# Performance work log

Measured on AMD Instinct MI355X. Metric: run time of the kernel, lower is better.

## Reference

```python
import jax, jax.numpy as jnp
import numpy as np
from jax import lax

BLOCK_LEN = 128  # ctx_len 8192 / blocks 64
NEG_INF = -1e9


def setup_inputs() -> dict:
    key = jax.random.key(0)
    ks = jax.random.split(key, 8)
    N, L, Dm = 2, 8192, 4096
    W, H, dh = 1024, 16, 64  # width = d_model*0.25
    s = lambda fan: 1.0 / np.sqrt(fan)
    return {
        "inputs": jax.random.normal(ks[0], (N, L, Dm), jnp.float32),
        "conv_w": jax.random.normal(ks[1], (3, Dm, 3 * W), jnp.float32) * s(3 * Dm),
        "conv_b": jnp.zeros((3 * W,), jnp.float32),
        "wq": jax.random.normal(ks[2], (W, H, dh), jnp.float32) * s(W),
        "bq": jnp.zeros((H, dh), jnp.float32),
        "wk": jax.random.normal(ks[3], (W, H, dh), jnp.float32) * s(W),
        "bk": jnp.zeros((H, dh), jnp.float32),
        "wv": jax.random.normal(ks[4], (W, H, dh), jnp.float32) * s(W),
        "bv": jnp.zeros((H, dh), jnp.float32),
        "wo": jax.random.normal(ks[5], (H, dh, W), jnp.float32) * s(H * dh),
        "bo": jnp.zeros((W,), jnp.float32),
        "proj_w": jax.random.normal(ks[6], (W, Dm), jnp.float32) * s(W),
        "proj_b": jnp.zeros((Dm,), jnp.float32),
    }


def reference(inputs, conv_w, conv_b, wq, bq, wk, bk, wv, bv, wo, bo, proj_w, proj_b):
    N, L, Dm = inputs.shape
    # Conv1D(kernel=3, same padding) producing q,k,v concatenated
    x = lax.conv_general_dilated(
        inputs, conv_w, window_strides=(1,), padding="SAME",
        dimension_numbers=("NWC", "WIO", "NWC")) + conv_b
    q, k, v = jnp.split(x, 3, axis=-1)  # each [N, L, W]
    W_ = q.shape[-1]
    nb = L // BLOCK_LEN
    # row attention: independent causal attention within each block
    q = q.reshape(N * nb, BLOCK_LEN, W_)
    k = k.reshape(N * nb, BLOCK_LEN, W_)
    v = v.reshape(N * nb, BLOCK_LEN, W_)
    dh = wq.shape[-1]
    qh = jnp.einsum("btd,dhe->bthe", q, wq) + bq  # [B, T, H, dh]
    kh = jnp.einsum("btd,dhe->bthe", k, wk) + bk
    vh = jnp.einsum("btd,dhe->bthe", v, wv) + bv
    scale = 1.0 / jnp.sqrt(jnp.asarray(dh, qh.dtype))
    scores = jnp.einsum("bqhe,bkhe->bhqk", qh * scale, kh)
    causal = jnp.tril(jnp.ones((BLOCK_LEN, BLOCK_LEN), bool))
    scores = jnp.where(causal, scores, NEG_INF)
    p = jax.nn.softmax(scores, axis=-1)
    o = jnp.einsum("bhqk,bkhe->bqhe", p, vh)
    o = jnp.einsum("bqhe,hed->bqd", o, wo) + bo  # MHA output projection -> width
    o = o.reshape(N, L, W_)
    return o @ proj_w + proj_b  # final Dense(d_model)
```

## Files before the change

### kernel.cpp

```cpp
#include <hip/hip_runtime.h>
#include <hip/hip_bf16.h>
#include <stdint.h>

typedef __attribute__((ext_vector_type(8))) short short8;
typedef __attribute__((ext_vector_type(4))) float f32x4;

#define AS1 __attribute__((address_space(1)))
#define AS3 __attribute__((address_space(3)))

__device__ __forceinline__ short f2bf(float x) {
    __hip_bfloat16 h = __float2bfloat16(x);
    union { __hip_bfloat16 h; short s; } u; u.h = h; return u.s;
}

__device__ __forceinline__ void gload_lds16(const short* g, short* l) {
    __builtin_amdgcn_global_load_lds((const AS1 void*)g, (AS3 void*)l, 16, 0, 0);
}

#define SBAR()   __builtin_amdgcn_s_barrier()
#define WAITV(N) asm volatile("s_waitcnt vmcnt(" #N ")")
#define SCHED0() __builtin_amdgcn_sched_barrier(0)

__global__ __launch_bounds__(256, 3) void conv3_gemm(
    const short* __restrict__ A,
    const short* __restrict__ BT,
    short* __restrict__ Cout,
    const float* __restrict__ bias)
{
    __shared__ __align__(16) short As[258 * 32];
    __shared__ __align__(16) short Bs[3 * 128 * 32];
    const int tid = threadIdx.x, lane = tid & 63, wid = tid >> 6;
    const int wm = wid >> 1, wn = wid & 1;
    const int m0 = blockIdx.y * 256, n0 = blockIdx.x * 128;
    const size_t arow0 = (size_t)(m0 >> 13) * 8194 + (size_t)(m0 & 8191);
    const short* Abase = A + arow0 * 4096;
    const short* Bbase = BT + (size_t)n0 * 4096;
    const int c15 = lane & 15, g = lane >> 4, g4 = g * 4;
    const int xr0 = (c15 >> 1) & 3;
    const int xr1 = ((c15 + 1) >> 1) & 3;
    const int xr2 = ((c15 + 2) >> 1) & 3;
    const int srow = tid >> 2;
    const int schunk = (((tid & 3) ^ ((tid >> 3) & 3)) * 8);
    const int srowB = wid * 32 + (lane >> 2);
    const int schunkB = (((lane & 3) ^ ((lane >> 3) & 3)) * 8);

#define STAGE(s) do { \
    const int kc_ = (s) * 32; \
    const short* ga_ = Abase + (size_t)srow * 4096 + kc_ + schunk; \
    short* la_ = As + wid * 512; \
    gload_lds16(ga_, la_); \
    gload_lds16(ga_ + (size_t)64 * 4096, la_ + 2048); \
    gload_lds16(ga_ + (size_t)128 * 4096, la_ + 4096); \
    gload_lds16(ga_ + (size_t)192 * 4096, la_ + 6144); \
    if (wid == 3 && lane < 8) \
        gload_lds16(Abase + (size_t)(256 + (lane >> 2)) * 4096 + kc_ + (lane & 3) * 8, \
                    As + 8192); \
    _Pragma("unroll") \
    for (int tp_ = 0; tp_ < 3; ++tp_) { \
        const short* gb_ = Bbase + (size_t)tp_ * 3072 * 4096 \
                           + (size_t)srowB * 4096 + kc_ + schunkB; \
        short* lb_ = Bs + tp_ * 4096 + wid * 1024; \
        gload_lds16(gb_, lb_); \
        gload_lds16(gb_ + (size_t)16 * 4096, lb_ + 512); \
    } \
} while (0)

#define LDA_T(mi, T, XR) (*(const short8*)(As \
    + (wm * 128 + (mi) * 16 + c15 + (T)) * 32 + ((g ^ (XR)) * 8)))
#define LDB_T(tp, nj) (*(const short8*)(Bs + (tp) * 4096 \
    + (wn * 64 + (nj) * 16 + c15) * 32 + ((g ^ xr0) * 8)))

    f32x4 acc[8][4];
    #pragma unroll
    for (int i = 0; i < 8; ++i)
        #pragma unroll
        for (int j = 0; j < 4; ++j)
            acc[i][j] = (f32x4){0.f, 0.f, 0.f, 0.f};

    STAGE(0);

    for (int s = 0; s < 128; ++s) {
        WAITV(0); SBAR(); SCHED0();
        #pragma unroll
        for (int tp = 0; tp < 3; ++tp) {
            const int xr = (tp == 0) ? xr0 : (tp == 1) ? xr1 : xr2;
            short8 b0 = LDB_T(tp, 0), b1 = LDB_T(tp, 1);
            short8 b2f = LDB_T(tp, 2), b3 = LDB_T(tp, 3);
            __builtin_amdgcn_s_setprio(1);
            #pragma unroll
            for (int mi = 0; mi < 8; ++mi) {
                short8 a = LDA_T(mi, tp, xr);
                acc[mi][0] = __builtin_amdgcn_mfma_f32_16x16x32_bf16(a, b0, acc[mi][0], 0, 0, 0);
                acc[mi][1] = __builtin_amdgcn_mfma_f32_16x16x32_bf16(a, b1, acc[mi][1], 0, 0, 0);
                acc[mi][2] = __builtin_amdgcn_mfma_f32_16x16x32_bf16(a, b2f, acc[mi][2], 0, 0, 0);
                acc[mi][3] = __builtin_amdgcn_mfma_f32_16x16x32_bf16(a, b3, acc[mi][3], 0, 0, 0);
            }
            __builtin_amdgcn_s_setprio(0);
        }
        SBAR();
        if (s + 1 < 128) STAGE(s + 1);
    }

    float bv[4];
    #pragma unroll
    for (int nj = 0; nj < 4; ++nj)
        bv[nj] = bias[n0 + wn * 64 + nj * 16 + c15];
    #pragma unroll
    for (int mi = 0; mi < 8; ++mi) {
        #pragma unroll
        for (int r = 0; r < 4; ++r) {
            const size_t row = (size_t)m0 + wm * 128 + mi * 16 + g4 + r;
            #pragma unroll
            for (int nj = 0; nj < 4; ++nj) {
                const int col = n0 + wn * 64 + nj * 16 + c15;
                Cout[row * 3072 + col] = f2bf(acc[mi][nj][r] + bv[nj]);
            }
        }
    }
#undef STAGE
#undef LDA_T
#undef LDB_T
}

template<int MODE, bool F32OUT>
__global__ __launch_bounds__(512, 2) void gemm256(
    const short* __restrict__ A, int lda,
    const short* __restrict__ BT, int ldb,
    void* __restrict__ Cout, int ldc,
    const float* __restrict__ bias, int Ktiles)
{
    __shared__ __align__(16) short As[2 * 2 * 256 * 32];
    __shared__ __align__(16) short Bs[2 * 2 * 256 * 32];
    const int tid = threadIdx.x, lane = tid & 63, wid = tid >> 6;
    const int wm = wid >> 2, wn = wid & 3;
    const int m0 = blockIdx.y * 256, n0 = blockIdx.x * 256;
    const size_t ldaS = (size_t)lda, ldbS = (size_t)ldb;
    const short* Abase0 = A + (size_t)m0 * ldaS;
    const short* Bbase0 = BT + (size_t)n0 * ldbS + ((MODE == 1) ? (m0 & ~1023) : 0);
    const int c15 = lane & 15, g4 = (lane >> 4) * 4;
    const int swz = ((lane >> 4) ^ ((c15 >> 1) & 3)) * 8;
    const int srow = tid >> 2;
    const int schunk = (((tid & 3) ^ ((tid >> 3) & 3)) * 8);

#define STG_A(u, kh, buf) do { \
    const short* g_ = Abase0 + ((u) << 6) + (kh) * 32 + (size_t)srow * ldaS + schunk; \
    short* l_ = As + (buf) * 16384 + (kh) * 8192 + wid * 512; \
    gload_lds16(g_, l_); \
    gload_lds16(g_ + 128 * ldaS, l_ + 4096); \
} while (0)

#define STG_B(u, kh, buf) do { \
    const short* g_ = Bbase0 + ((u) << 6) + (kh) * 32 + (size_t)srow * ldbS + schunk; \
    short* l_ = Bs + (buf) * 16384 + (kh) * 8192 + wid * 512; \
    gload_lds16(g_, l_); \
    gload_lds16(g_ + 128 * ldbS, l_ + 4096); \
} while (0)

#define LDA_(buf, kk, mi) (*(const short8*)(As + (buf) * 16384 + (kk) * 8192 \
                           + (wm * 128 + (mi) * 16 + c15) * 32 + swz))
#define LDB_(buf, kk, nj) (*(const short8*)(Bs + (buf) * 16384 + (kk) * 8192 \
                           + (wn * 64 + (nj) * 16 + c15) * 32 + swz))

#define MFMA4x4(MB) do { \
    __builtin_amdgcn_s_setprio(1); \
    _Pragma("unroll") \
    for (int mi_ = 0; mi_ < 4; ++mi_) \
        _Pragma("unroll") \
        for (int nj_ = 0; nj_ < 4; ++nj_) \
            acc[(MB) + mi_][nj_] = __builtin_amdgcn_mfma_f32_16x16x32_bf16( \
                af[mi_], bf4[nj_], acc[(MB) + mi_][nj_], 0, 0, 0); \
    __builtin_amdgcn_s_setprio(0); \
} while (0)

    f32x4 acc[8][4];
    #pragma unroll
    for (int i = 0; i < 8; ++i)
        #pragma unroll
        for (int j = 0; j < 4; ++j)
            acc[i][j] = (f32x4){0.f, 0.f, 0.f, 0.f};

    STG_A(0, 0, 0); STG_B(0, 0, 0); STG_A(0, 1, 0); STG_B(0, 1, 0);
    WAITV(4); SBAR(); SCHED0();

    for (int t = 0; t < Ktiles; ++t) {
        const int c = t & 1, nb = c ^ 1;
        const bool st = (t + 1 < Ktiles);
        const int u = t + 1;
        short8 af[4], bf4[4];

        #pragma unroll
        for (int mi = 0; mi < 4; ++mi) af[mi] = LDA_(c, 0, mi);
        #pragma unroll
        for (int nj = 0; nj < 4; ++nj) bf4[nj] = LDB_(c, 0, nj);
        if (st) STG_A(u, 0, nb);
        SBAR();
        MFMA4x4(0);
        SBAR();

        #pragma unroll
        for (int mi = 0; mi < 4; ++mi) af[mi] = LDA_(c, 0, 4 + mi);
        if (st) STG_B(u, 0, nb);
        if (st) { WAITV(4); } else { WAITV(0); }
        SBAR(); SCHED0();
        MFMA4x4(4);
        SBAR();

        #pragma unroll
        for (int mi = 0; mi < 4; ++mi) af[mi] = LDA_(c, 1, mi);
        #pragma unroll
        for (int nj = 0; nj < 4; ++nj) bf4[nj] = LDB_(c, 1, nj);
        if (st) STG_A(u, 1, nb);
        SBAR();
        MFMA4x4(0);
        SBAR();

        #pragma unroll
        for (int mi = 0; mi < 4; ++mi) af[mi] = LDA_(c, 1, 4 + mi);
        if (st) STG_B(u, 1, nb);
        if (st) { WAITV(4); } else { WAITV(0); }
        SBAR(); SCHED0();
        MFMA4x4(4);
        SBAR();
    }

    float bv[4];
    #pragma unroll
    for (int nj = 0; nj < 4; ++nj)
        bv[nj] = bias ? bias[n0 + wn * 64 + nj * 16 + c15] : 0.f;
    #pragma unroll
    for (int mi = 0; mi < 8; ++mi) {
        #pragma unroll
        for (int r = 0; r < 4; ++r) {
            const size_t row = (size_t)m0 + wm * 128 + mi * 16 + g4 + r;
            #pragma unroll
            for (int nj = 0; nj < 4; ++nj) {
                const int col = n0 + wn * 64 + nj * 16 + c15;
                const float v = acc[mi][nj][r] + bv[nj];
                if (F32OUT) ((float*)Cout)[row * (size_t)ldc + col] = v;
                else        ((short*)Cout)[row * (size_t)ldc + col] = f2bf(v);
            }
        }
    }
#undef STG_A
#undef STG_B
#undef LDA_
#undef LDB_
#undef MFMA4x4
}

__global__ __launch_bounds__(256) void attn_kernel(
    const short* __restrict__ qkvh, short* __restrict__ obuf)
{
    __shared__ __align__(16) char smem[54272];
    short* qs = (short*)smem;
    short* ks = (short*)smem + 9216;
    short* vt = (short*)(smem + 36864);
    short* ps = (short*)smem;
    short* os = (short*)smem;

    const int tid = threadIdx.x, lane = tid & 63, wid = tid >> 6;
    const int h = blockIdx.x, b = blockIdx.y;
    const size_t base = (size_t)b * 128 * 3072 + (size_t)h * 64;

    for (int i = tid; i < 1024; i += 256) {
        const int row = i >> 3, c8 = i & 7;
        const size_t g = base + (size_t)row * 3072 + c8 * 8;
        *(short8*)(qs + row * 72 + c8 * 8) = *(const short8*)(qkvh + g);
        *(short8*)(ks + row * 72 + c8 * 8) = *(const short8*)(qkvh + g + 1024);
        short8 vv = *(const short8*)(qkvh + g + 2048);
        #pragma unroll
        for (int j = 0; j < 8; ++j) vt[(c8 * 8 + j) * 136 + row] = vv[j];
    }
    __syncthreads();

    const int c15 = lane & 15, g8 = (lane >> 4) * 8, g4 = (lane >> 4) * 4;
    const int r0 = wid * 32;

    f32x4 sacc[2][8];
    #pragma unroll
    for (int mi = 0; mi < 2; ++mi)
        #pragma unroll
        for (int nj = 0; nj < 8; ++nj)
            sacc[mi][nj] = (f32x4){0.f, 0.f, 0.f, 0.f};
    #pragma unroll
    for (int kk = 0; kk < 2; ++kk) {
        short8 aq[2];
        #pragma unroll
        for (int mi = 0; mi < 2; ++mi)
            aq[mi] = *(const short8*)(qs + (r0 + mi * 16 + c15) * 72 + kk * 32 + g8);
        #pragma unroll
        for (int nj = 0; nj < 8; ++nj) {
            short8 bk8 = *(const short8*)(ks + (nj * 16 + c15) * 72 + kk * 32 + g8);
            #pragma unroll
            for (int mi = 0; mi < 2; ++mi)
                sacc[mi][nj] = __builtin_amdgcn_mfma_f32_16x16x32_bf16(
                    aq[mi], bk8, sacc[mi][nj], 0, 0, 0);
        }
    }
    __syncthreads();

    #pragma unroll
    for (int mi = 0; mi < 2; ++mi) {
        #pragma unroll
        for (int r = 0; r < 4; ++r) {
            const int qrow = r0 + mi * 16 + g4 + r;
            float m = -3.0e38f, pv[8];
            #pragma unroll
            for (int nj = 0; nj < 8; ++nj) {
                float s = sacc[mi][nj][r] * 0.125f;
                if (nj * 16 + c15 > qrow) s = -1.0e9f;
                pv[nj] = s; m = fmaxf(m, s);
            }
            #pragma unroll
            for (int off = 8; off >= 1; off >>= 1) m = fmaxf(m, __shfl_xor(m, off));
            float sum = 0.f;
            #pragma unroll
            for (int nj = 0; nj < 8; ++nj) { float p = __expf(pv[nj] - m); pv[nj] = p; sum += p; }
            #pragma unroll
            for (int off = 8; off >= 1; off >>= 1) sum += __shfl_xor(sum, off);
            const float inv = 1.0f / sum;
            #pragma unroll
            for (int nj = 0; nj < 8; ++nj)
                ps[qrow * 136 + nj * 16 + c15] = f2bf(pv[nj] * inv);
        }
    }
    __syncthreads();

    f32x4 oacc[2][4];
    #pragma unroll
    for (int mi = 0; mi < 2; ++mi)
        #pragma unroll
        for (int nj = 0; nj < 4; ++nj)
            oacc[mi][nj] = (f32x4){0.f, 0.f, 0.f, 0.f};
    #pragma unroll
    for (int kt = 0; kt < 4; ++kt) {
        short8 ap[2];
        #pragma unroll
        for (int mi = 0; mi < 2; ++mi)
            ap[mi] = *(const short8*)(ps + (r0 + mi * 16 + c15) * 136 + kt * 32 + g8);
        #pragma unroll
        for (int nj = 0; nj < 4; ++nj) {
            short8 bv8 = *(const short8*)(vt + (nj * 16 + c15) * 136 + kt * 32 + g8);
            #pragma unroll
            for (int mi = 0; mi < 2; ++mi)
                oacc[mi][nj] = __builtin_amdgcn_mfma_f32_16x16x32_bf16(
                    ap[mi], bv8, oacc[mi][nj], 0, 0, 0);
        }
    }
    __syncthreads();

    #pragma unroll
    for (int mi = 0; mi < 2; ++mi)
        #pragma unroll
        for (int r = 0; r < 4; ++r)
            #pragma unroll
            for (int nj = 0; nj < 4; ++nj)
                os[(r0 + mi * 16 + g4 + r) * 72 + nj * 16 + c15] = f2bf(oacc[mi][nj][r]);
    __syncthreads();

    for (int i = tid; i < 1024; i += 256) {
        const int row = i >> 3, c8 = i & 7;
        *(short8*)(obuf + (size_t)b * 128 * 1024 + (size_t)h * 64
                   + (size_t)row * 1024 + c8 * 8) =
            *(const short8*)(os + row * 72 + c8 * 8);
    }
}

__global__ void pad_convert_inputs(const float* __restrict__ in, short* __restrict__ out)
{
    const int row = blockIdx.x;
    const int n = row / 8194, l = row % 8194;
    short* orow = out + (size_t)row * 4096;
    if (l == 0 || l == 8193) {
        for (int i = threadIdx.x; i < 512; i += 256) {
            uint4 z; z.x = z.y = z.z = z.w = 0u;
            *(uint4*)(orow + i * 8) = z;
        }
    } else {
        const float* irow = in + ((size_t)n * 8192 + (l - 1)) * 4096;
        for (int i = threadIdx.x; i < 512; i += 256) {
            float4 a = *(const float4*)(irow + i * 8);
            float4 b = *(const float4*)(irow + i * 8 + 4);
            short8 v;
            v[0] = f2bf(a.x); v[1] = f2bf(a.y); v[2] = f2bf(a.z); v[3] = f2bf(a.w);
            v[4] = f2bf(b.x); v[5] = f2bf(b.y); v[6] = f2bf(b.z); v[7] = f2bf(b.w);
            *(short8*)(orow + i * 8) = v;
        }
    }
}

__global__ void transpose_convert(const float* __restrict__ in, short* __restrict__ out,
                                  int R, int C)
{
    __shared__ float tile[32][33];
    const int tx = threadIdx.x & 31, ty = threadIdx.x >> 5;
    const int bx = blockIdx.x * 32, by = blockIdx.y * 32;
    #pragma unroll
    for (int i = 0; i < 32; i += 8)
        tile[ty + i][tx] = in[(size_t)(by + ty + i) * C + bx + tx];
    __syncthreads();
    #pragma unroll
    for (int i = 0; i < 32; i += 8)
        out[(size_t)(bx + ty + i) * R + by + tx] = f2bf(tile[tx][ty + i]);
}

__global__ void convert_bf16(const float* __restrict__ in, short* __restrict__ out, int n8)
{
    const int idx = blockIdx.x * 256 + threadIdx.x;
    if (idx < n8) {
        float4 a = *(const float4*)(in + (size_t)idx * 8);
        float4 b = *(const float4*)(in + (size_t)idx * 8 + 4);
        short8 v;
        v[0] = f2bf(a.x); v[1] = f2bf(a.y); v[2] = f2bf(a.z); v[3] = f2bf(a.w);
        v[4] = f2bf(b.x); v[5] = f2bf(b.y); v[6] = f2bf(b.z); v[7] = f2bf(b.w);
        *(short8*)(out + (size_t)idx * 8) = v;
    }
}

__global__ void fuse_bias(const float* __restrict__ bo, const float* __restrict__ projw,
                          const float* __restrict__ projb, float* __restrict__ outb)
{
    const int j = blockIdx.x * 256 + threadIdx.x;
    float s = projb[j];
    for (int w = 0; w < 1024; ++w) s = fmaf(bo[w], projw[(size_t)w * 4096 + j], s);
    outb[j] = s;
}

__global__ void fuse_bias_qkv(const float* __restrict__ conv_b,
                              const float* __restrict__ wq, const float* __restrict__ bq,
                              const float* __restrict__ wk, const float* __restrict__ bk,
                              const float* __restrict__ wv, const float* __restrict__ bv,
                              float* __restrict__ outb)
{
    const int o = blockIdx.x * 256 + threadIdx.x;
    const int p = o >> 10, e = o & 1023;
    const float* w = (p == 0) ? wq : (p == 1) ? wk : wv;
    const float* bb = (p == 0) ? bq : (p == 1) ? bk : bv;
    const float* cb = conv_b + p * 1024;
    float s = bb[e];
    for (int d = 0; d < 1024; ++d) s = fmaf(cb[d], w[(size_t)d * 1024 + e], s);
    outb[o] = s;
}

extern "C" void kernel_launch(void* const* d_in, const int* in_sizes, int n_in,
                              void* d_out, int out_size, void* d_ws, size_t ws_size,
                              hipStream_t stream)
{
    const float* inputs = (const float*)d_in[0];
    const float* conv_w = (const float*)d_in[1];
    const float* conv_b = (const float*)d_in[2];
    const float* wq     = (const float*)d_in[3];
    const float* bq     = (const float*)d_in[4];
    const float* wk     = (const float*)d_in[5];
    const float* bk     = (const float*)d_in[6];
    const float* wv     = (const float*)d_in[7];
    const float* bv     = (const float*)d_in[8];
    const float* wo     = (const float*)d_in[9];
    const float* bo     = (const float*)d_in[10];
    const float* proj_w = (const float*)d_in[11];
    const float* proj_b = (const float*)d_in[12];

    char* ws = (char*)d_ws;
    short* in_pad = (short*)(ws + 0);
    short* cw_bf  = (short*)(ws + 134283264);
    short* qkvh   = (short*)(ws + 134283264);
    short* W2T    = (short*)(ws + 234946560);
    short* wq_t   = (short*)(ws + 310444032);
    short* wo_bf  = (short*)(ws + 316735488);
    short* proj_t = (short*)(ws + 318832640);
    short* WfT    = (short*)(ws + 327221248);
    float* bfused = (float*)(ws + 335609856);
    float* b2     = (float*)(ws + 335626240);
    short* o_buf  = (short*)(ws + 0);

    dim3 blk(256), blk5(512);

    pad_convert_inputs<<<16388, blk, 0, stream>>>(inputs, in_pad);
    convert_bf16<<<18432, blk, 0, stream>>>(conv_w, cw_bf, 4718592);
    transpose_convert<<<dim3(32, 32), blk, 0, stream>>>(wq, wq_t, 1024, 1024);
    transpose_convert<<<dim3(32, 32), blk, 0, stream>>>(wk, wq_t + 1048576, 1024, 1024);
    transpose_convert<<<dim3(32, 32), blk, 0, stream>>>(wv, wq_t + 2097152, 1024, 1024);
    transpose_convert<<<dim3(128, 32), blk, 0, stream>>>(proj_w, proj_t, 1024, 4096);
    convert_bf16<<<512, blk, 0, stream>>>(wo, wo_bf, 131072);
    fuse_bias<<<16, blk, 0, stream>>>(bo, proj_w, proj_b, bfused);
    fuse_bias_qkv<<<12, blk, 0, stream>>>(conv_b, wq, bq, wk, bk, wv, bv, b2);

    gemm256<0, false><<<dim3(4, 16), blk5, 0, stream>>>(
        proj_t, 1024, wo_bf, 1024, WfT, 1024, nullptr, 16);
    for (int t = 0; t < 3; ++t)
        gemm256<1, false><<<dim3(16, 12), blk5, 0, stream>>>(
            wq_t, 1024, cw_bf + (size_t)t * 4096 * 3072, 3072,
            W2T + (size_t)t * 3072 * 4096, 4096, nullptr, 16);
    conv3_gemm<<<dim3(24, 64), blk, 0, stream>>>(in_pad, W2T, qkvh, b2);

    attn_kernel<<<dim3(16, 128), blk, 0, stream>>>(qkvh, o_buf);

    gemm256<0, true><<<dim3(16, 64), blk5, 0, stream>>>(
        o_buf, 1024, WfT, 1024, d_out, 4096, bfused, 16);
}
```

Baseline: 1.494 ms.

## Replace 256x256 double-buffered GEMM with 256x128 single-buffered 4-wave GEMM

The 512-thread, 256x256-tile, double-buffered GEMM is replaced by a 256-thread kernel with 256x128 tiles and a single LDS buffer per 32-wide K step. Each step waits for the load, computes 32 MFMAs per wave, then issues the next load, so load and compute no longer overlap inside a block. The aim is smaller LDS use, more blocks in flight and more tiles for load balance, with latency hidden by other resident blocks rather than the software pipeline. The risks are exposed load latency and more global traffic for B from the narrower N tile.

```diff
diff --git a/kernel.cpp b/kernel.cpp
--- a/kernel.cpp
+++ b/kernel.cpp
@@ -123,54 +123,43 @@
 }
 
 template<int MODE, bool F32OUT>
-__global__ __launch_bounds__(512, 2) void gemm256(
+__global__ __launch_bounds__(256, 3) void gemm128(
     const short* __restrict__ A, int lda,
     const short* __restrict__ BT, int ldb,
     void* __restrict__ Cout, int ldc,
-    const float* __restrict__ bias, int Ktiles)
-{
-    __shared__ __align__(16) short As[2 * 2 * 256 * 32];
-    __shared__ __align__(16) short Bs[2 * 2 * 256 * 32];
+    const float* __restrict__ bias, int Ksteps)
+{
+    __shared__ __align__(16) short As[256 * 32];
+    __shared__ __align__(16) short Bs[128 * 32];
     const int tid = threadIdx.x, lane = tid & 63, wid = tid >> 6;
-    const int wm = wid >> 2, wn = wid & 3;
-    const int m0 = blockIdx.y * 256, n0 = blockIdx.x * 256;
+    const int wm = wid >> 1, wn = wid & 1;
+    const int m0 = blockIdx.y * 256, n0 = blockIdx.x * 128;
     const size_t ldaS = (size_t)lda, ldbS = (size_t)ldb;
-    const short* Abase0 = A + (size_t)m0 * ldaS;
-    const short* Bbase0 = BT + (size_t)n0 * ldbS + ((MODE == 1) ? (m0 & ~1023) : 0);
-    const int c15 = lane & 15, g4 = (lane >> 4) * 4;
-    const int swz = ((lane >> 4) ^ ((c15 >> 1) & 3)) * 8;
+    const short* Abase = A + (size_t)m0 * ldaS;
+    const short* Bbase = BT + (size_t)n0 * ldbS + ((MODE == 1) ? (m0 & ~1023) : 0);
+    const int c15 = lane & 15, g = lane >> 4, g4 = g * 4;
+    const int xr0 = (c15 >> 1) & 3;
     const int srow = tid >> 2;
     const int schunk = (((tid & 3) ^ ((tid >> 3) & 3)) * 8);
-
-#define STG_A(u, kh, buf) do { \
-    const short* g_ = Abase0 + ((u) << 6) + (kh) * 32 + (size_t)srow * ldaS + schunk; \
-    short* l_ = As + (buf) * 16384 + (kh) * 8192 + wid * 512; \
-    gload_lds16(g_, l_); \
-    gload_lds16(g_ + 128 * ldaS, l_ + 4096); \
+    const int srowB = wid * 32 + (lane >> 2);
+    const int schunkB = (((lane & 3) ^ ((lane >> 3) & 3)) * 8);
+
+#define STG(s) do { \
+    const int kc_ = (s) * 32; \
+    const short* ga_ = Abase + (size_t)srow * ldaS + kc_ + schunk; \
+    short* la_ = As + wid * 512; \
+    gload_lds16(ga_, la_); \
+    gload_lds16(ga_ + (size_t)64 * ldaS, la_ + 2048); \
+    gload_lds16(ga_ + (size_t)128 * ldaS, la_ + 4096); \
+    gload_lds16(ga_ + (size_t)192 * ldaS, la_ + 6144); \
+    const short* gb_ = Bbase + (size_t)srowB * ldbS + kc_ + schunkB; \
+    short* lb_ = Bs + wid * 1024; \
+    gload_lds16(gb_, lb_); \
+    gload_lds16(gb_ + (size_t)16 * ldbS, lb_ + 512); \
 } while (0)
 
-#define STG_B(u, kh, buf) do { \
-    const short* g_ = Bbase0 + ((u) << 6) + (kh) * 32 + (size_t)srow * ldbS + schunk; \
-    short* l_ = Bs + (buf) * 16384 + (kh) * 8192 + wid * 512; \
-    gload_lds16(g_, l_); \
-    gload_lds16(g_ + 128 * ldbS, l_ + 4096); \
-} while (0)
-
-#define LDA_(buf, kk, mi) (*(const short8*)(As + (buf) * 16384 + (kk) * 8192 \
-                           + (wm * 128 + (mi) * 16 + c15) * 32 + swz))
-#define LDB_(buf, kk, nj) (*(const short8*)(Bs + (buf) * 16384 + (kk) * 8192 \
-                           + (wn * 64 + (nj) * 16 + c15) * 32 + swz))
-
-#define MFMA4x4(MB) do { \
-    __builtin_amdgcn_s_setprio(1); \
-    _Pragma("unroll") \
-    for (int mi_ = 0; mi_ < 4; ++mi_) \
-        _Pragma("unroll") \
-        for (int nj_ = 0; nj_ < 4; ++nj_) \
-            acc[(MB) + mi_][nj_] = __builtin_amdgcn_mfma_f32_16x16x32_bf16( \
-                af[mi_], bf4[nj_], acc[(MB) + mi_][nj_], 0, 0, 0); \
-    __builtin_amdgcn_s_setprio(0); \
-} while (0)
+#define LDA_(mi) (*(const short8*)(As + (wm * 128 + (mi) * 16 + c15) * 32 + ((g ^ xr0) * 8)))
+#define LDB_(nj) (*(const short8*)(Bs + (wn * 64 + (nj) * 16 + c15) * 32 + ((g ^ xr0) * 8)))
 
     f32x4 acc[8][4];
     #pragma unroll
@@ -179,48 +168,23 @@
         for (int j = 0; j < 4; ++j)
             acc[i][j] = (f32x4){0.f, 0.f, 0.f, 0.f};
 
-    STG_A(0, 0, 0); STG_B(0, 0, 0); STG_A(0, 1, 0); STG_B(0, 1, 0);
-    WAITV(4); SBAR(); SCHED0();
-
-    for (int t = 0; t < Ktiles; ++t) {
-        const int c = t & 1, nb = c ^ 1;
-        const bool st = (t + 1 < Ktiles);
-        const int u = t + 1;
-        short8 af[4], bf4[4];
-
-        #pragma unroll
-        for (int mi = 0; mi < 4; ++mi) af[mi] = LDA_(c, 0, mi);
-        #pragma unroll
-        for (int nj = 0; nj < 4; ++nj) bf4[nj] = LDB_(c, 0, nj);
-        if (st) STG_A(u, 0, nb);
+    STG(0);
+
+    for (int s = 0; s < Ksteps; ++s) {
+        WAITV(0); SBAR(); SCHED0();
+        short8 b0 = LDB_(0), b1 = LDB_(1), b2f = LDB_(2), b3 = LDB_(3);
+        __builtin_amdgcn_s_setprio(1);
+        #pragma unroll
+        for (int mi = 0; mi < 8; ++mi) {
+            short8 a = LDA_(mi);
+            acc[mi][0] = __builtin_amdgcn_mfma_f32_16x16x32_bf16(a, b0, acc[mi][0], 0, 0, 0);
+            acc[mi][1] = __builtin_amdgcn_mfma_f32_16x16x32_bf16(a, b1, acc[mi][1], 0, 0, 0);
+            acc[mi][2] = __builtin_amdgcn_mfma_f32_16x16x32_bf16(a, b2f, acc[mi][2], 0, 0, 0);
+            acc[mi][3] = __builtin_amdgcn_mfma_f32_16x16x32_bf16(a, b3, acc[mi][3], 0, 0, 0);
+        }
+        __builtin_amdgcn_s_setprio(0);
         SBAR();
-        MFMA4x4(0);
-        SBAR();
-
-        #pragma unroll
-        for (int mi = 0; mi < 4; ++mi) af[mi] = LDA_(c, 0, 4 + mi);
-        if (st) STG_B(u, 0, nb);
-        if (st) { WAITV(4); } else { WAITV(0); }
-        SBAR(); SCHED0();
-        MFMA4x4(4);
-        SBAR();
-
-        #pragma unroll
-        for (int mi = 0; mi < 4; ++mi) af[mi] = LDA_(c, 1, mi);
-        #pragma unroll
-        for (int nj = 0; nj < 4; ++nj) bf4[nj] = LDB_(c, 1, nj);
-        if (st) STG_A(u, 1, nb);
-        SBAR();
-        MFMA4x4(0);
-        SBAR();
-
-        #pragma unroll
-        for (int mi = 0; mi < 4; ++mi) af[mi] = LDA_(c, 1, 4 + mi);
-        if (st) STG_B(u, 1, nb);
-        if (st) { WAITV(4); } else { WAITV(0); }
-        SBAR(); SCHED0();
-        MFMA4x4(4);
-        SBAR();
+        if (s + 1 < Ksteps) STG(s + 1);
     }
 
     float bv[4];
@@ -241,11 +205,9 @@
             }
         }
     }
-#undef STG_A
-#undef STG_B
+#undef STG
 #undef LDA_
 #undef LDB_
-#undef MFMA4x4
 }
 
 __global__ __launch_bounds__(256) void attn_kernel(
@@ -473,7 +435,7 @@
     float* b2     = (float*)(ws + 335626240);
     short* o_buf  = (short*)(ws + 0);
 
-    dim3 blk(256), blk5(512);
+    dim3 blk(256);
 
     pad_convert_inputs<<<16388, blk, 0, stream>>>(inputs, in_pad);
     convert_bf16<<<18432, blk, 0, stream>>>(conv_w, cw_bf, 4718592);
@@ -485,16 +447,16 @@
     fuse_bias<<<16, blk, 0, stream>>>(bo, proj_w, proj_b, bfused);
     fuse_bias_qkv<<<12, blk, 0, stream>>>(conv_b, wq, bq, wk, bk, wv, bv, b2);
 
-    gemm256<0, false><<<dim3(4, 16), blk5, 0, stream>>>(
-        proj_t, 1024, wo_bf, 1024, WfT, 1024, nullptr, 16);
+    gemm128<0, false><<<dim3(8, 16), blk, 0, stream>>>(
+        proj_t, 1024, wo_bf, 1024, WfT, 1024, nullptr, 32);
     for (int t = 0; t < 3; ++t)
-        gemm256<1, false><<<dim3(16, 12), blk5, 0, stream>>>(
+        gemm128<1, false><<<dim3(32, 12), blk, 0, stream>>>(
             wq_t, 1024, cw_bf + (size_t)t * 4096 * 3072, 3072,
-            W2T + (size_t)t * 3072 * 4096, 4096, nullptr, 16);
+            W2T + (size_t)t * 3072 * 4096, 4096, nullptr, 32);
     conv3_gemm<<<dim3(24, 64), blk, 0, stream>>>(in_pad, W2T, qkvh, b2);
 
     attn_kernel<<<dim3(16, 128), blk, 0, stream>>>(qkvh, o_buf);
 
-    gemm256<0, true><<<dim3(16, 64), blk5, 0, stream>>>(
-        o_buf, 1024, WfT, 1024, d_out, 4096, bfused, 16);
-}
+    gemm128<0, true><<<dim3(32, 64), blk, 0, stream>>>(
+        o_buf, 1024, WfT, 1024, d_out, 4096, bfused, 32);
+}
```

Measured after the change: 1.514 ms (median of 2 runs). No clear change (+1.3%).
